# Performance work log

Hardware: AMD Instinct MI355X
Metric: run time of the kernel (lower is better)

## Reference

```python
import jax, jax.numpy as jnp
import numpy as np

N_NODES = 100000
N_EDGES = 1600000
D_IN = 128
D_OUT = 128


def setup_inputs() -> dict:
    key = jax.random.key(0)
    k_x, k_e, k_wl, k_bl, k_wr = jax.random.split(key, 5)
    x = jax.random.normal(k_x, (N_NODES, D_IN), dtype=jnp.float32)
    edge_index = jax.random.randint(k_e, (2, N_EDGES), 0, N_NODES, dtype=jnp.int64)
    s = 1.0 / np.sqrt(D_IN)
    W_l = jax.random.uniform(k_wl, (D_OUT, D_IN), minval=-s, maxval=s, dtype=jnp.float32)
    b_l = jax.random.uniform(k_bl, (D_OUT,), minval=-s, maxval=s, dtype=jnp.float32)
    W_r = jax.random.uniform(k_wr, (D_OUT, D_IN), minval=-s, maxval=s, dtype=jnp.float32)
    return {"x": x, "edge_index": edge_index, "W_l": W_l, "b_l": b_l, "W_r": W_r}


def reference(x, edge_index, W_l, b_l, W_r):
    # PyG SAGEConv with mean aggregation:
    #   out = lin_l(mean_{j in N(i)} x_j) + lin_r(x_i), followed by ReLU.
    src, dst = edge_index[0], edge_index[1]
    # gather source features [E, D_IN] and mean-aggregate at destinations
    msg_sum = jax.ops.segment_sum(x[src], dst, num_segments=N_NODES)  # [N, D_IN]
    deg = jax.ops.segment_sum(jnp.ones((edge_index.shape[1],), dtype=x.dtype), dst,
                              num_segments=N_NODES)  # [N]
    agg = msg_sum / jnp.maximum(deg, 1.0)[:, None]  # isolated nodes -> 0
    out = agg @ W_l.T + b_l + x @ W_r.T
    return jax.nn.relu(out)
```

## Files before the change

### kernel.cpp

```cpp
#include <hip/hip_runtime.h>
#include <hip/hip_bf16.h>
#include <cstddef>
#include <cstdint>

#define D 128
#define BCHUNK 2048
#define SLOTS 64
#define QTILE 64
#define LROW 68
#define SBCAP 5120
#define NGMAX 512

typedef __bf16 bf16x8 __attribute__((ext_vector_type(8)));
typedef float  f32x4  __attribute__((ext_vector_type(4)));
typedef float  f32x2  __attribute__((ext_vector_type(2)));

__device__ __forceinline__ unsigned int f2bf(float f) {
    unsigned int u = __float_as_uint(f);
    return (u + 0x7FFFu + ((u >> 16) & 1u)) >> 16;
}

__global__ __launch_bounds__(256) void bucketx2_kernel(
    const int* __restrict__ ei, int E, int* __restrict__ subCnt,
    unsigned int* __restrict__ sub, int NG, int nbE, int nbX,
    const float4* __restrict__ x4, uint2* __restrict__ xb2,
    unsigned int* __restrict__ xg, int nq,
    const float* __restrict__ Wl, const float* __restrict__ Wr,
    const float* __restrict__ bl, unsigned short* __restrict__ bfrag,
    float* __restrict__ biasbuf)
{
    const int bid = blockIdx.x;
    if (bid >= nbE) {
        const int xi = bid - nbE;
        if (xi < nbX) {
            const int base = xi * 1024 + threadIdx.x;
            #pragma unroll
            for (int k = 0; k < 4; k++) {
                int i = base + k * 256;
                if (i < nq) {
                    float4 v = x4[i];
                    uint2 r;
                    r.x = f2bf(v.x) | (f2bf(v.y) << 16);
                    r.y = f2bf(v.z) | (f2bf(v.w) << 16);
                    xb2[i] = r;
                    int g = 0;
                    g = __builtin_amdgcn_cvt_pk_fp8_f32(v.x, v.y, g, false);
                    g = __builtin_amdgcn_cvt_pk_fp8_f32(v.z, v.w, g, true);
                    xg[(size_t)((i >> 5) + 1) * 32 + (i & 31)] = (unsigned int)g;
                }
            }
        } else {
            int f = (xi - nbX) * 256 + threadIdx.x;
            if (f < 4096) {
                int ct   = f >> 9;
                int q    = (f >> 6) & 7;
                int lane = f & 63;
                int o  = 16 * ct + (lane & 15);
                int kb = 32 * q + (lane >> 4) * 8;
                const float* s = (kb < 128) ? (Wl + (size_t)o * 128 + kb)
                                            : (Wr + (size_t)o * 128 + (kb - 128));
                uint4 u;
                u.x = f2bf(s[0]) | (f2bf(s[1]) << 16);
                u.y = f2bf(s[2]) | (f2bf(s[3]) << 16);
                u.z = f2bf(s[4]) | (f2bf(s[5]) << 16);
                u.w = f2bf(s[6]) | (f2bf(s[7]) << 16);
                reinterpret_cast<uint4*>(bfrag)[f] = u;
                if (f < 128) biasbuf[f] = bl[f];
                if (f < 32)  xg[f] = 0u;
            }
        }
        return;
    }
    __shared__ int cnt[NGMAX], base[NGMAX];
    for (int i = threadIdx.x; i < NG; i += 256) cnt[i] = 0;
    __syncthreads();
    const int cb = bid * BCHUNK;
    int srcs[8], gs[8], d8s[8];
    #pragma unroll
    for (int k = 0; k < 8; k++) {
        int e = cb + threadIdx.x + k * 256;
        bool v = e < E;
        srcs[k] = v ? ei[e] : 0;
        int dst = v ? ei[E + e] : 0;
        gs[k]  = v ? (dst >> 8) : -1;
        d8s[k] = dst & 255;
        if (v) atomicAdd(&cnt[gs[k]], 1);
    }
    __syncthreads();
    for (int i = threadIdx.x; i < NG; i += 256)
        base[i] = (cnt[i] > 0) ? atomicAdd(&subCnt[i], cnt[i]) : 0;
    __syncthreads();
    #pragma unroll
    for (int k = 0; k < 8; k++) {
        if (gs[k] >= 0) {
            int pos = atomicAdd(&base[gs[k]], 1);
            if (pos < SBCAP)
                sub[(size_t)gs[k] * SBCAP + pos] =
                    (unsigned int)(srcs[k] + 1) | ((unsigned int)d8s[k] << 20);
        }
    }
}

__global__ __launch_bounds__(512) void gathformer_kernel(
    const unsigned int* __restrict__ sub, const int* __restrict__ subCnt,
    const unsigned int* __restrict__ xg, const unsigned int* __restrict__ xb,
    const unsigned short* __restrict__ bfrag, const float* __restrict__ biasbuf,
    float* __restrict__ out, int N)
{
    __shared__ unsigned int lds[QTILE * LROW];
    __shared__ int lcsr[QTILE * SLOTS];
    __shared__ int lcnt[QTILE];

    const int g     = blockIdx.x >> 2;
    const int h     = blockIdx.x & 3;
    const int node0 = (g << 8) + (h << 6);

    const int w    = threadIdx.x >> 6;
    const int lane = threadIdx.x & 63;
    const int sb   = lane & 31;
    const int half = lane >> 5;

    if (threadIdx.x < QTILE) lcnt[threadIdx.x] = 0;
    __syncthreads();
    const int n = min(subCnt[g], SBCAP);
    const unsigned int* S = sub + (size_t)g * SBCAP;
    for (int i = threadIdx.x; i < n; i += 512) {
        unsigned int en = S[i];
        int d8 = (en >> 20) & 255;
        if ((d8 >> 6) == h) {
            int ln  = d8 & 63;
            int pos = atomicAdd(&lcnt[ln], 1);
            if (pos < SLOTS) lcsr[ln * SLOTS + pos] = (int)(en & 0xFFFFFu);
        }
    }
    __syncthreads();

    for (int i = 0; i < 8; i++) {
        int ln   = w * 8 + i;
        int node = node0 + ln;
        if (node >= N) break;
        int deg = lcnt[ln];
        int dl  = min(deg, SLOTS);
        int nbatch = (dl + 15) >> 4;
        const int* nb = lcsr + ln * SLOTS;
        f32x2 a01 = {0.f, 0.f};
        f32x2 a23 = {0.f, 0.f};
        for (int b = 0; b < nbatch; b++) {
            const int j = b * 16;
            unsigned int v[8];
            #pragma unroll
            for (int u = 0; u < 8; u++) {
                int slot = j + 2 * u + half;
                int raw  = nb[slot];
                int s    = (slot < dl) ? raw : 0;
                v[u] = xg[(size_t)s * 32 + sb];
            }
            #pragma unroll
            for (int u = 0; u < 8; u++) {
                a01 += __builtin_amdgcn_cvt_pk_f32_fp8(v[u], false);
                a23 += __builtin_amdgcn_cvt_pk_f32_fp8(v[u], true);
            }
        }
        a01.x += __shfl_xor(a01.x, 32);
        a01.y += __shfl_xor(a01.y, 32);
        a23.x += __shfl_xor(a23.x, 32);
        a23.y += __shfl_xor(a23.y, 32);
        if (half == 0) {
            float inv = 1.0f / fmaxf((float)deg, 1.0f);
            int b = ln * LROW + sb * 2;
            lds[b]     = f2bf(a01.x * inv) | (f2bf(a01.y * inv) << 16);
            lds[b + 1] = f2bf(a23.x * inv) | (f2bf(a23.y * inv) << 16);
        }
    }
    __syncthreads();

    const int quad = lane >> 4;
    const int r15  = lane & 15;
    bf16x8 bw[8];
    #pragma unroll
    for (int q = 0; q < 8; q++)
        bw[q] = reinterpret_cast<const bf16x8*>(bfrag)[(w * 8 + q) * 64 + lane];
    const float bias = biasbuf[16 * w + r15];
    const int col = 16 * w + r15;

    #pragma unroll 1
    for (int mt = 0; mt < 4; mt++) {
        int rowbase = node0 + mt * 16;
        if (rowbase >= N) break;
        int rc = min(rowbase + r15, N - 1);
        f32x4 acc = {0.f, 0.f, 0.f, 0.f};
        const int lbase = (mt * 16 + r15) * LROW + quad * 4;
        #pragma unroll
        for (int q = 0; q < 4; q++) {
            bf16x8 a = *reinterpret_cast<const bf16x8*>(&lds[lbase + q * 16]);
            acc = __builtin_amdgcn_mfma_f32_16x16x32_bf16(a, bw[q], acc, 0, 0, 0);
        }
        const unsigned short* xrow =
            (const unsigned short*)xb + (size_t)rc * 128 + quad * 8;
        #pragma unroll
        for (int q = 4; q < 8; q++) {
            bf16x8 a = *reinterpret_cast<const bf16x8*>(xrow + (q - 4) * 32);
            acc = __builtin_amdgcn_mfma_f32_16x16x32_bf16(a, bw[q], acc, 0, 0, 0);
        }
        #pragma unroll
        for (int r = 0; r < 4; r++) {
            int orow = rowbase + quad * 4 + r;
            if (orow < N)
                out[(size_t)orow * D + col] = fmaxf(acc[r] + bias, 0.0f);
        }
    }
}

extern "C" void kernel_launch(void* const* d_in, const int* in_sizes, int n_in,
                              void* d_out, int out_size, void* d_ws, size_t ws_size,
                              hipStream_t stream)
{
    const float* x  = (const float*)d_in[0];
    const int*   ei = (const int*)d_in[1];
    const float* Wl = (const float*)d_in[2];
    const float* bl = (const float*)d_in[3];
    const float* Wr = (const float*)d_in[4];
    float* out = (float*)d_out;

    const int nodes = in_sizes[0] / D;
    const int E     = in_sizes[1] / 2;
    const int NG    = (nodes + 255) >> 8;

    unsigned int* xg = (unsigned int*)d_ws;
    unsigned int* xb = xg + (size_t)(nodes + 1) * 32;
    unsigned short* bfrag = (unsigned short*)(xb + (size_t)nodes * 64);
    float* biasbuf   = (float*)(bfrag + 4096 * 8);
    int* subCnt      = (int*)(biasbuf + 128);
    unsigned int* sub = (unsigned int*)(subCnt + 512);

    hipMemsetAsync(subCnt, 0, (size_t)NG * sizeof(int), stream);

    const int nbE = (E + BCHUNK - 1) / BCHUNK;
    const int nq  = nodes * 32;
    const int nbX = (nq + 1023) / 1024;
    bucketx2_kernel<<<nbE + nbX + 16, 256, 0, stream>>>(
        ei, E, subCnt, sub, NG, nbE, nbX,
        (const float4*)x, (uint2*)xb, xg, nq, Wl, Wr, bl, bfrag, biasbuf);

    gathformer_kernel<<<NG * 4, 512, 0, stream>>>(
        sub, subCnt, xg, xb, bfrag, biasbuf, out, nodes);
}
```

Baseline: 195.2 us.

## Widen dst buckets to 512 nodes, double edge chunk, vectorize bucket scan

Destination buckets grow from 256 to 512 nodes, which halves the bucket count and the number of global atomics per chunk. Each bucketing block now handles 4096 edges, and each block of the gather kernel scans a bucket that is twice as large with uint4 loads. The per-node loop gets a precomputed trip count and is unrolled by 2. In exchange, each of the 8 sub-blocks re-reads and filters the whole bucket, so redundant reading of bucket entries doubles (8 blocks scanning ~6400 entries instead of 4 scanning ~3200). The uint4 loads also assume the bucket base stays 16-byte aligned, which holds because 9728 is a multiple of 4.

```diff
diff --git a/kernel.cpp b/kernel.cpp
--- a/kernel.cpp
+++ b/kernel.cpp
@@ -4,12 +4,13 @@
 #include <cstdint>
 
 #define D 128
-#define BCHUNK 2048
+#define BCHUNK 4096
 #define SLOTS 64
 #define QTILE 64
 #define LROW 68
-#define SBCAP 5120
-#define NGMAX 512
+#define GRAN 512
+#define SBCAP 9728
+#define NGMAX 256
 
 typedef __bf16 bf16x8 __attribute__((ext_vector_type(8)));
 typedef float  f32x4  __attribute__((ext_vector_type(4)));
@@ -75,15 +76,15 @@
     for (int i = threadIdx.x; i < NG; i += 256) cnt[i] = 0;
     __syncthreads();
     const int cb = bid * BCHUNK;
-    int srcs[8], gs[8], d8s[8];
+    int srcs[16], gs[16], d9s[16];
     #pragma unroll
-    for (int k = 0; k < 8; k++) {
+    for (int k = 0; k < 16; k++) {
         int e = cb + threadIdx.x + k * 256;
         bool v = e < E;
         srcs[k] = v ? ei[e] : 0;
         int dst = v ? ei[E + e] : 0;
-        gs[k]  = v ? (dst >> 8) : -1;
-        d8s[k] = dst & 255;
+        gs[k]  = v ? (dst >> 9) : -1;
+        d9s[k] = dst & 511;
         if (v) atomicAdd(&cnt[gs[k]], 1);
     }
     __syncthreads();
@@ -91,12 +92,12 @@
         base[i] = (cnt[i] > 0) ? atomicAdd(&subCnt[i], cnt[i]) : 0;
     __syncthreads();
     #pragma unroll
-    for (int k = 0; k < 8; k++) {
+    for (int k = 0; k < 16; k++) {
         if (gs[k] >= 0) {
             int pos = atomicAdd(&base[gs[k]], 1);
             if (pos < SBCAP)
                 sub[(size_t)gs[k] * SBCAP + pos] =
-                    (unsigned int)(srcs[k] + 1) | ((unsigned int)d8s[k] << 20);
+                    (unsigned int)(srcs[k] + 1) | ((unsigned int)d9s[k] << 20);
         }
     }
 }
@@ -111,9 +112,9 @@
     __shared__ int lcsr[QTILE * SLOTS];
     __shared__ int lcnt[QTILE];
 
-    const int g     = blockIdx.x >> 2;
-    const int h     = blockIdx.x & 3;
-    const int node0 = (g << 8) + (h << 6);
+    const int g     = blockIdx.x >> 3;
+    const int h     = blockIdx.x & 7;
+    const int node0 = g * GRAN + (h << 6);
 
     const int w    = threadIdx.x >> 6;
     const int lane = threadIdx.x & 63;
@@ -124,21 +125,27 @@
     __syncthreads();
     const int n = min(subCnt[g], SBCAP);
     const unsigned int* S = sub + (size_t)g * SBCAP;
-    for (int i = threadIdx.x; i < n; i += 512) {
-        unsigned int en = S[i];
-        int d8 = (en >> 20) & 255;
-        if ((d8 >> 6) == h) {
-            int ln  = d8 & 63;
-            int pos = atomicAdd(&lcnt[ln], 1);
-            if (pos < SLOTS) lcsr[ln * SLOTS + pos] = (int)(en & 0xFFFFFu);
-        }
-    }
-    __syncthreads();
-
-    for (int i = 0; i < 8; i++) {
-        int ln   = w * 8 + i;
-        int node = node0 + ln;
-        if (node >= N) break;
+    for (int bi = (int)threadIdx.x * 4; bi < n; bi += 2048) {
+        uint4 e4 = *reinterpret_cast<const uint4*>(S + bi);
+        #pragma unroll
+        for (int j = 0; j < 4; j++) {
+            unsigned int en = (&e4.x)[j];
+            if (bi + j < n) {
+                int d9 = (en >> 20) & 511;
+                if ((d9 >> 6) == h) {
+                    int ln  = d9 & 63;
+                    int pos = atomicAdd(&lcnt[ln], 1);
+                    if (pos < SLOTS) lcsr[ln * SLOTS + pos] = (int)(en & 0xFFFFFu);
+                }
+            }
+        }
+    }
+    __syncthreads();
+
+    const int imax = min(8, N - node0 - w * 8);
+    #pragma unroll 2
+    for (int i = 0; i < imax; i++) {
+        int ln  = w * 8 + i;
         int deg = lcnt[ln];
         int dl  = min(deg, SLOTS);
         int nbatch = (dl + 15) >> 4;
@@ -224,7 +231,7 @@
 
     const int nodes = in_sizes[0] / D;
     const int E     = in_sizes[1] / 2;
-    const int NG    = (nodes + 255) >> 8;
+    const int NG    = (nodes + GRAN - 1) / GRAN;
 
     unsigned int* xg = (unsigned int*)d_ws;
     unsigned int* xb = xg + (size_t)(nodes + 1) * 32;
@@ -242,6 +249,6 @@
         ei, E, subCnt, sub, NG, nbE, nbX,
         (const float4*)x, (uint2*)xb, xg, nq, Wl, Wr, bl, bfrag, biasbuf);
 
-    gathformer_kernel<<<NG * 4, 512, 0, stream>>>(
+    gathformer_kernel<<<NG * 8, 512, 0, stream>>>(
         sub, subCnt, xg, xb, bfrag, biasbuf, out, nodes);
 }
```

Result: faster. 188.0 us (-3.7%).
